# Kernel tuning notes

Hardware: AMD Instinct MI355X
Metric: run time of the kernel (lower is better)

## Reference

```python
import jax, jax.numpy as jnp
import numpy as np
import math

N_HEAD = 16
NEG = -1e30  # stands in for -inf in masked_fill; identical post-softmax


def setup_inputs() -> dict:
    key = jax.random.key(0)
    ks = jax.random.split(key, 8)
    B, S, D = 4, 2048, 1024
    x = jax.random.normal(ks[0], (B, S, D), dtype=jnp.float32)
    mask = jax.random.randint(ks[1], (B, S), 0, 2).astype(jnp.int32)
    qmask = jax.random.randint(ks[2], (B, S), 0, 2).astype(jnp.int32)
    w_qkv = jax.random.normal(ks[3], (3 * D, D), dtype=jnp.float32) / math.sqrt(D)
    w_fc = jax.random.normal(ks[4], (D, D), dtype=jnp.float32) / math.sqrt(D)
    b_fc = jax.random.normal(ks[5], (D,), dtype=jnp.float32) * 0.01
    # shift = abs(randn)+0.001 (positive), bias = -abs(randn) (negative)
    shift = jnp.abs(jax.random.normal(ks[6], (1,), dtype=jnp.float32)) + 0.001
    bias_p = -jnp.abs(jax.random.normal(ks[7], (1,), dtype=jnp.float32))
    return {"x": x, "mask": mask, "qmask": qmask, "use_Gaussian": 1,
            "w_qkv": w_qkv, "w_fc": w_fc, "b_fc": b_fc,
            "shift": shift, "bias_p": bias_p}


def reference(x, mask, qmask, use_Gaussian, w_qkv, w_fc, b_fc, shift, bias_p):
    B, S, D = x.shape
    H = N_HEAD
    Dh = D // H
    scale = math.sqrt(Dh)
    qkv = jnp.einsum('bsd,ed->bse', x, w_qkv)  # [B,S,3D]
    q, k, v = jnp.split(qkv, 3, axis=-1)
    q = q.reshape(B, S, H, Dh).transpose(0, 2, 1, 3)  # [B,H,S,Dh]
    k = k.reshape(B, S, H, Dh).transpose(0, 2, 1, 3)
    v = v.reshape(B, S, H, Dh).transpose(0, 2, 1, 3)
    attn = jnp.einsum('bhqd,bhkd->bhqk', q, k) / scale
    key_mask = (mask != 0)[:, None, None, :]  # [B,1,1,S]
    attn = jnp.where(key_mask, attn, NEG)
    if use_Gaussian:
        idx = jnp.arange(S, dtype=jnp.float32)
        sq_dist = (idx[:, None] - idx[None, :]) ** 2  # (i-j)^2 == H+H.T-2G
        dis = -(shift[0] * sq_dist + bias_p[0])  # [S,S]
        attn = attn + dis[None, None]
    attn = jax.nn.softmax(attn, axis=-1)
    out = jnp.einsum('bhqk,bhkd->bhqd', attn, v)
    out = out.transpose(0, 2, 1, 3).reshape(B, S, D)
    return jnp.einsum('bsd,ed->bse', out, w_fc) + b_fc
```

## Files before the change

kernel.cpp:

```cpp
#include <hip/hip_runtime.h>
#include <hip/hip_bf16.h>
#include <stdint.h>
#include <math.h>

#define DI __device__ __forceinline__

typedef unsigned short u16;
typedef __bf16   bf16x8 __attribute__((ext_vector_type(8)));
typedef float    f32x4  __attribute__((ext_vector_type(4)));

#define BSZ 4
#define SEQ 2048
#define DMODEL 1024
#define NHEAD 16
#define DHEAD 64

DI u16 f2b(float f) {
    uint32_t u = __float_as_uint(f);
    u += 0x7fffu + ((u >> 16) & 1u);
    return (u16)(u >> 16);
}

DI uint32_t f2b2(float a, float b) {
    __hip_bfloat162 h = __float22bfloat162_rn(float2{a, b});
    uint32_t u; __builtin_memcpy(&u, &h, 4); return u;
}

DI void async16(const void* g, void* l) {
    __builtin_amdgcn_global_load_lds(
        (const __attribute__((address_space(1))) void*)g,
        (__attribute__((address_space(3))) void*)l, 16, 0, 0);
}

__global__ __launch_bounds__(256) void cast_all(
    const float* __restrict__ x,  const float* __restrict__ wq,
    const float* __restrict__ wf, u16* __restrict__ xb,
    u16* __restrict__ wqb, u16* __restrict__ wfb)
{
    const int idx = blockIdx.x * 256 + threadIdx.x;
    const float* src; u16* dst; int off;
    if (idx < 2097152)      { src = x;  dst = xb;  off = idx; }
    else if (idx < 2883584) { src = wq; dst = wqb; off = idx - 2097152; }
    else                    { src = wf; dst = wfb; off = idx - 2883584; }
    const int i = off * 4;
    f32x4 v = *(const f32x4*)(src + i);
    *(uint2*)(dst + i) = make_uint2(f2b2(v[0], v[1]), f2b2(v[2], v[3]));
}

__global__ __launch_bounds__(256) void gemm_qkv(
    const u16* __restrict__ A, const u16* __restrict__ Bm, int K,
    u16* __restrict__ qb, u16* __restrict__ kb, u16* __restrict__ vb)
{
    __shared__ u16 As[128 * 64];
    __shared__ u16 Bs[128 * 64];

    const int tid  = threadIdx.x;
    const int l    = tid & 63, w = tid >> 6;
    const int quad = l >> 4, lc = l & 15;
    const int wm   = w >> 1, wn = w & 1;
    const int m0   = blockIdx.y * 128, n0 = blockIdx.x * 128;

    f32x4 acc[4][4];
#pragma unroll
    for (int i = 0; i < 4; i++)
#pragma unroll
        for (int j = 0; j < 4; j++) acc[i][j] = (f32x4){0.f, 0.f, 0.f, 0.f};

    const int  srow   = tid >> 3;
    const int  schunk = (tid & 7) ^ (srow & 7);
    const size_t aBase = (size_t)(m0 + srow) * K + schunk * 8;
    const size_t bBase = (size_t)(n0 + srow) * K + schunk * 8;

    for (int k0 = 0; k0 < K; k0 += 64) {
        __syncthreads();
#pragma unroll
        for (int i = 0; i < 4; i++) {
            async16(A  + aBase + (size_t)(32 * i) * K + k0, As + i * 2048 + w * 512);
            async16(Bm + bBase + (size_t)(32 * i) * K + k0, Bs + i * 2048 + w * 512);
        }
        __syncthreads();

#pragma unroll
        for (int kh = 0; kh < 2; kh++) {
            bf16x8 af[4], bf[4];
            const int g = kh * 4 + quad;
#pragma unroll
            for (int mi = 0; mi < 4; mi++) {
                const int mr = wm * 64 + mi * 16 + lc;
                af[mi] = *(const bf16x8*)&As[mr * 64 + ((g ^ (mr & 7)) * 8)];
            }
#pragma unroll
            for (int ni = 0; ni < 4; ni++) {
                const int nr = wn * 64 + ni * 16 + lc;
                bf[ni] = *(const bf16x8*)&Bs[nr * 64 + ((g ^ (nr & 7)) * 8)];
            }
#pragma unroll
            for (int mi = 0; mi < 4; mi++)
#pragma unroll
                for (int ni = 0; ni < 4; ni++)
                    acc[mi][ni] = __builtin_amdgcn_mfma_f32_16x16x32_bf16(
                        af[mi], bf[ni], acc[mi][ni], 0, 0, 0);
        }
    }

#pragma unroll
    for (int mi = 0; mi < 4; mi++) {
        const int mrow = m0 + wm * 64 + mi * 16 + quad * 4;
#pragma unroll
        for (int ni = 0; ni < 4; ni++) {
            const int e = n0 + wn * 64 + ni * 16 + lc;
#pragma unroll
            for (int r = 0; r < 4; r++) {
                const int m = mrow + r;
                const int part = e >> 10, rem = e & 1023;
                const int h = rem >> 6, dh = rem & 63;
                const int b = m >> 11, s = m & 2047;
                u16* dst = (part == 0) ? qb : ((part == 1) ? kb : vb);
                dst[(((size_t)(b * NHEAD + h) * SEQ + s) << 6) + dh] = f2b(acc[mi][ni][r]);
            }
        }
    }
}

__global__ __launch_bounds__(256) void gemm_fc(
    const u16* __restrict__ A, const u16* __restrict__ Bm, int K,
    const float* __restrict__ bias, float* __restrict__ outF, int N)
{
    __shared__ u16 As[2][128 * 64];
    __shared__ u16 Bs[2][128 * 64];

    const int tid  = threadIdx.x;
    const int l    = tid & 63, w = tid >> 6;
    const int quad = l >> 4, lc = l & 15;
    const int wm   = w >> 1, wn = w & 1;
    const int m0   = blockIdx.y * 128, n0 = blockIdx.x * 128;

    f32x4 acc[4][4];
#pragma unroll
    for (int i = 0; i < 4; i++)
#pragma unroll
        for (int j = 0; j < 4; j++) acc[i][j] = (f32x4){0.f, 0.f, 0.f, 0.f};

    const int  srow   = tid >> 3;
    const int  schunk = (tid & 7) ^ (srow & 7);
    const size_t aBase = (size_t)(m0 + srow) * K + schunk * 8;
    const size_t bBase = (size_t)(n0 + srow) * K + schunk * 8;

    const int NT = K / 64;

#pragma unroll
    for (int i = 0; i < 4; i++) {
        async16(A  + aBase + (size_t)(32 * i) * K, As[0] + i * 2048 + w * 512);
        async16(Bm + bBase + (size_t)(32 * i) * K, Bs[0] + i * 2048 + w * 512);
    }
    __syncthreads();

    for (int kt = 0; kt < NT; ++kt) {
        const int cur = kt & 1;
        if (kt + 1 < NT) {
            const int nxt = (kt + 1) & 1;
            const int k0  = (kt + 1) * 64;
#pragma unroll
            for (int i = 0; i < 4; i++) {
                async16(A  + aBase + (size_t)(32 * i) * K + k0, As[nxt] + i * 2048 + w * 512);
                async16(Bm + bBase + (size_t)(32 * i) * K + k0, Bs[nxt] + i * 2048 + w * 512);
            }
        }

#pragma unroll
        for (int kh = 0; kh < 2; kh++) {
            bf16x8 af[4], bf[4];
            const int g = kh * 4 + quad;
#pragma unroll
            for (int mi = 0; mi < 4; mi++) {
                const int mr = wm * 64 + mi * 16 + lc;
                af[mi] = *(const bf16x8*)&As[cur][mr * 64 + ((g ^ (mr & 7)) * 8)];
            }
#pragma unroll
            for (int ni = 0; ni < 4; ni++) {
                const int nr = wn * 64 + ni * 16 + lc;
                bf[ni] = *(const bf16x8*)&Bs[cur][nr * 64 + ((g ^ (nr & 7)) * 8)];
            }
#pragma unroll
            for (int mi = 0; mi < 4; mi++)
#pragma unroll
                for (int ni = 0; ni < 4; ni++)
                    acc[mi][ni] = __builtin_amdgcn_mfma_f32_16x16x32_bf16(
                        af[mi], bf[ni], acc[mi][ni], 0, 0, 0);
        }
        __syncthreads();
    }

#pragma unroll
    for (int mi = 0; mi < 4; mi++) {
        const int mrow = m0 + wm * 64 + mi * 16 + quad * 4;
#pragma unroll
        for (int ni = 0; ni < 4; ni++) {
            const int e = n0 + wn * 64 + ni * 16 + lc;
            const float be = bias[e];
#pragma unroll
            for (int r = 0; r < 4; r++)
                outF[(size_t)(mrow + r) * N + e] = acc[mi][ni][r] + be;
        }
    }
}

#define PST 72
__global__ __launch_bounds__(256) void attn_kernel(
    const u16* __restrict__ Q, const u16* __restrict__ Kg, const u16* __restrict__ Vg,
    const int* __restrict__ mask, const int* __restrict__ gaussp,
    const float* __restrict__ shiftp, const float* __restrict__ biaspp,
    u16* __restrict__ outA)
{
    __shared__ u16 Ks[8 * 64 * 8];
    __shared__ u16 Vt[64 * PST];
    __shared__ u16 Ps[64 * PST];

    const int tid  = threadIdx.x;
    const int l    = tid & 63, w = tid >> 6;
    const int quad = l >> 4, lc = l & 15;
    const int qt = blockIdx.x, h = blockIdx.y, b = blockIdx.z;
    const int bh = b * NHEAD + h;
    const int q0 = qt * 64;

    const float shift = shiftp[0];
    const float biasp = biaspp[0];
    const int   gauss = gaussp[0];

    const u16* Qbase = Q  + ((size_t)bh * SEQ << 6);
    const u16* Kbase = Kg + ((size_t)bh * SEQ << 6);
    const u16* Vbase = Vg + ((size_t)bh * SEQ << 6);
    const int* mbase = mask + b * SEQ;

    int kt_lo = 0, kt_hi = SEQ / 64 - 1;
    if (gauss) {
        const int dwin = (int)__fsqrt_rn(30.0f / shift) + 1;
        int lo = q0 - dwin;          if (lo < 0) lo = 0;
        int hi = q0 + 63 + dwin;     if (hi > SEQ - 1) hi = SEQ - 1;
        kt_lo = lo >> 6;
        kt_hi = hi >> 6;
    }

    bf16x8 qf[2];
#pragma unroll
    for (int ks = 0; ks < 2; ks++)
        qf[ks] = *(const bf16x8*)(Qbase +
            ((size_t)(q0 + w * 16 + lc) << 6) + ks * 32 + quad * 8);

    f32x4 oacc[4];
#pragma unroll
    for (int dt = 0; dt < 4; dt++) oacc[dt] = (f32x4){0.f, 0.f, 0.f, 0.f};
    float lsum[4];
#pragma unroll
    for (int r = 0; r < 4; r++) lsum[r] = 0.f;

    for (int kt = kt_lo; kt <= kt_hi; ++kt) {
        const int kk0 = kt * 64;
        __syncthreads();

        async16(Kbase + (size_t)(kk0 + l) * 64 + w * 8,       Ks + w * 512);
        async16(Kbase + (size_t)(kk0 + l) * 64 + (4 + w) * 8, Ks + 2048 + w * 512);

        {
            const u16* vg = Vbase + (size_t)(kk0 + l) * 64 + w * 16;
            bf16x8 v0 = *(const bf16x8*)vg;
            bf16x8 v1 = *(const bf16x8*)(vg + 8);
            const u16* v0b = (const u16*)&v0;
            const u16* v1b = (const u16*)&v1;
#pragma unroll
            for (int j = 0; j < 8; j++) Vt[(w * 16 + j) * PST + l] = v0b[j];
#pragma unroll
            for (int j = 0; j < 8; j++) Vt[(w * 16 + 8 + j) * PST + l] = v1b[j];
        }
        __syncthreads();

        bf16x8 kf[4][2];
#pragma unroll
        for (int nt = 0; nt < 4; nt++)
#pragma unroll
            for (int ks = 0; ks < 2; ks++)
                kf[nt][ks] = *(const bf16x8*)&Ks[(ks * 4 + quad) * 512 + (nt * 16 + lc) * 8];

        f32x4 sf[4];
#pragma unroll
        for (int nt = 0; nt < 4; nt++) sf[nt] = (f32x4){0.f, 0.f, 0.f, 0.f};
#pragma unroll
        for (int nt = 0; nt < 4; nt++)
#pragma unroll
            for (int ks = 0; ks < 2; ks++)
                sf[nt] = __builtin_amdgcn_mfma_f32_16x16x32_bf16(
                    qf[ks], kf[nt][ks], sf[nt], 0, 0, 0);

        float madd[4]; float jj[4];
#pragma unroll
        for (int nt = 0; nt < 4; nt++) {
            const int j = kk0 + nt * 16 + lc;
            madd[nt] = mbase[j] ? 0.f : -1e30f;
            jj[nt] = (float)j;
        }
#pragma unroll
        for (int r = 0; r < 4; r++) {
            const float fi = (float)(q0 + w * 16 + quad * 4 + r);
            float p[4];
#pragma unroll
            for (int nt = 0; nt < 4; nt++) {
                float s = sf[nt][r] * 0.125f + madd[nt] - 8.0f;
                if (gauss) { const float d = fi - jj[nt]; s -= shift * d * d + biasp; }
                p[nt] = __expf(s);
            }
            lsum[r] += (p[0] + p[1]) + (p[2] + p[3]);
            const uint32_t p01 = f2b2(p[0], p[1]);
            const uint32_t p23 = f2b2(p[2], p[3]);
            u16* prow = &Ps[(w * 16 + quad * 4 + r) * PST + lc];
            prow[0]  = (u16)p01;  prow[16] = (u16)(p01 >> 16);
            prow[32] = (u16)p23;  prow[48] = (u16)(p23 >> 16);
        }

        bf16x8 pa[2], vf[4][2];
#pragma unroll
        for (int ks = 0; ks < 2; ks++)
            pa[ks] = *(const bf16x8*)&Ps[(w * 16 + lc) * PST + ks * 32 + quad * 8];
#pragma unroll
        for (int dt = 0; dt < 4; dt++)
#pragma unroll
            for (int ks = 0; ks < 2; ks++)
                vf[dt][ks] = *(const bf16x8*)&Vt[(dt * 16 + lc) * PST + ks * 32 + quad * 8];
#pragma unroll
        for (int dt = 0; dt < 4; dt++)
#pragma unroll
            for (int ks = 0; ks < 2; ks++)
                oacc[dt] = __builtin_amdgcn_mfma_f32_16x16x32_bf16(
                    pa[ks], vf[dt][ks], oacc[dt], 0, 0, 0);
    }

    float lrow[4];
#pragma unroll
    for (int r = 0; r < 4; r++) {
        float ts = lsum[r];
        ts += __shfl_xor(ts, 1);
        ts += __shfl_xor(ts, 2);
        ts += __shfl_xor(ts, 4);
        ts += __shfl_xor(ts, 8);
        lrow[r] = ts;
    }

#pragma unroll
    for (int dt = 0; dt < 4; dt++)
#pragma unroll
        for (int r = 0; r < 4; r++) {
            const int qg  = q0 + w * 16 + quad * 4 + r;
            const int col = h * 64 + dt * 16 + lc;
            const float v = oacc[dt][r] / lrow[r];
            outA[((size_t)(b * SEQ + qg) << 10) + col] = f2b(v);
        }
}

extern "C" void kernel_launch(void* const* d_in, const int* in_sizes, int n_in,
                              void* d_out, int out_size, void* d_ws, size_t ws_size,
                              hipStream_t stream)
{
    const float* x      = (const float*)d_in[0];
    const int*   mask   = (const int*)d_in[1];
    const int*   gaussp = (const int*)d_in[3];
    const float* w_qkv  = (const float*)d_in[4];
    const float* w_fc   = (const float*)d_in[5];
    const float* b_fc   = (const float*)d_in[6];
    const float* shiftp = (const float*)d_in[7];
    const float* biaspp = (const float*)d_in[8];
    float* out = (float*)d_out;

    char* ws = (char*)d_ws;
    u16* xb  = (u16*)(ws);
    u16* wqb = (u16*)(ws + 16777216);
    u16* wfb = (u16*)(ws + 23068672);
    u16* qb  = (u16*)(ws + 25165824);
    u16* kb  = (u16*)(ws + 41943040);
    u16* vb  = (u16*)(ws + 58720256);

    cast_all<<<12288, 256, 0, stream>>>(x, w_qkv, w_fc, xb, wqb, wfb);

    gemm_qkv<<<dim3(24, 64), 256, 0, stream>>>(xb, wqb, DMODEL, qb, kb, vb);

    attn_kernel<<<dim3(SEQ / 64, NHEAD, BSZ), 256, 0, stream>>>(
        qb, kb, vb, mask, gaussp, shiftp, biaspp, xb);

    gemm_fc<<<dim3(8, 64), 256, 0, stream>>>(xb, wfb, DMODEL, b_fc, out, DMODEL);
}
```

Baseline: 219.1 us.

## Double-buffer K/V tiles in attention kernel to overlap loads with compute

Adds ping-pong shared-memory buffers for K and transposed V. The next tile is prefetched with async K copies and V register loads while the current tile's QK and PV MFMAs run. The loop now needs one barrier per iteration instead of two. The cost is more LDS use, which may lower occupancy, and the V prefetch registers stay live across the compute.

```diff
diff --git a/kernel.cpp b/kernel.cpp
--- a/kernel.cpp
+++ b/kernel.cpp
@@ -212,8 +212,8 @@
     const float* __restrict__ shiftp, const float* __restrict__ biaspp,
     u16* __restrict__ outA)
 {
-    __shared__ u16 Ks[8 * 64 * 8];
-    __shared__ u16 Vt[64 * PST];
+    __shared__ u16 Ks[2][4096];
+    __shared__ u16 Vt[2][64 * PST];
     __shared__ u16 Ps[64 * PST];
 
     const int tid  = threadIdx.x;
@@ -254,32 +254,45 @@
 #pragma unroll
     for (int r = 0; r < 4; r++) lsum[r] = 0.f;
 
+    {
+        const int kk0 = kt_lo * 64;
+        async16(Kbase + (size_t)(kk0 + l) * 64 + w * 8,       Ks[0] + w * 512);
+        async16(Kbase + (size_t)(kk0 + l) * 64 + (4 + w) * 8, Ks[0] + 2048 + w * 512);
+        const u16* vg = Vbase + (size_t)(kk0 + l) * 64 + w * 16;
+        bf16x8 v0 = *(const bf16x8*)vg;
+        bf16x8 v1 = *(const bf16x8*)(vg + 8);
+        const u16* v0b = (const u16*)&v0;
+        const u16* v1b = (const u16*)&v1;
+#pragma unroll
+        for (int j = 0; j < 8; j++) Vt[0][(w * 16 + j) * PST + l] = v0b[j];
+#pragma unroll
+        for (int j = 0; j < 8; j++) Vt[0][(w * 16 + 8 + j) * PST + l] = v1b[j];
+    }
+    __syncthreads();
+
     for (int kt = kt_lo; kt <= kt_hi; ++kt) {
+        const int cur = (kt - kt_lo) & 1;
+        const int nxt = cur ^ 1;
+        const bool pre = (kt < kt_hi);
+
+        bf16x8 v0, v1;
+        if (pre) {
+            const int kk1 = (kt + 1) * 64;
+            async16(Kbase + (size_t)(kk1 + l) * 64 + w * 8,       Ks[nxt] + w * 512);
+            async16(Kbase + (size_t)(kk1 + l) * 64 + (4 + w) * 8, Ks[nxt] + 2048 + w * 512);
+            const u16* vg = Vbase + (size_t)(kk1 + l) * 64 + w * 16;
+            v0 = *(const bf16x8*)vg;
+            v1 = *(const bf16x8*)(vg + 8);
+        }
+
         const int kk0 = kt * 64;
-        __syncthreads();
-
-        async16(Kbase + (size_t)(kk0 + l) * 64 + w * 8,       Ks + w * 512);
-        async16(Kbase + (size_t)(kk0 + l) * 64 + (4 + w) * 8, Ks + 2048 + w * 512);
-
-        {
-            const u16* vg = Vbase + (size_t)(kk0 + l) * 64 + w * 16;
-            bf16x8 v0 = *(const bf16x8*)vg;
-            bf16x8 v1 = *(const bf16x8*)(vg + 8);
-            const u16* v0b = (const u16*)&v0;
-            const u16* v1b = (const u16*)&v1;
-#pragma unroll
-            for (int j = 0; j < 8; j++) Vt[(w * 16 + j) * PST + l] = v0b[j];
-#pragma unroll
-            for (int j = 0; j < 8; j++) Vt[(w * 16 + 8 + j) * PST + l] = v1b[j];
-        }
-        __syncthreads();
 
         bf16x8 kf[4][2];
 #pragma unroll
         for (int nt = 0; nt < 4; nt++)
 #pragma unroll
             for (int ks = 0; ks < 2; ks++)
-                kf[nt][ks] = *(const bf16x8*)&Ks[(ks * 4 + quad) * 512 + (nt * 16 + lc) * 8];
+                kf[nt][ks] = *(const bf16x8*)&Ks[cur][(ks * 4 + quad) * 512 + (nt * 16 + lc) * 8];
 
         f32x4 sf[4];
 #pragma unroll
@@ -324,13 +337,23 @@
         for (int dt = 0; dt < 4; dt++)
 #pragma unroll
             for (int ks = 0; ks < 2; ks++)
-                vf[dt][ks] = *(const bf16x8*)&Vt[(dt * 16 + lc) * PST + ks * 32 + quad * 8];
+                vf[dt][ks] = *(const bf16x8*)&Vt[cur][(dt * 16 + lc) * PST + ks * 32 + quad * 8];
 #pragma unroll
         for (int dt = 0; dt < 4; dt++)
 #pragma unroll
             for (int ks = 0; ks < 2; ks++)
                 oacc[dt] = __builtin_amdgcn_mfma_f32_16x16x32_bf16(
                     pa[ks], vf[dt][ks], oacc[dt], 0, 0, 0);
+
+        if (pre) {
+            const u16* v0b = (const u16*)&v0;
+            const u16* v1b = (const u16*)&v1;
+#pragma unroll
+            for (int j = 0; j < 8; j++) Vt[nxt][(w * 16 + j) * PST + l] = v0b[j];
+#pragma unroll
+            for (int j = 0; j < 8; j++) Vt[nxt][(w * 16 + 8 + j) * PST + l] = v1b[j];
+        }
+        __syncthreads();
     }
 
     float lrow[4];
```

New measurement: 223.3 us. About the same (+1.9%).
